# Kernel optimization log

Measured on AMD Instinct MI355X. Metric: run time of the kernel, lower is better.

## Reference

```python
import jax, jax.numpy as jnp
import numpy as np
from jax import lax


def conv3(x, w):
    # standard 3x3 conv, stride 1, pad 1, no bias (offset-predicting conv)
    return lax.conv_general_dilated(x, w, window_strides=(1, 1),
                                    padding=((1, 1), (1, 1)),
                                    dimension_numbers=('NCHW', 'OIHW', 'NCHW'))


def deform_conv(x, offset, weight, bias, groups):
    # torchvision.ops.DeformConv2d semantics, kernel 3x3, stride 1, pad 1,
    # dilation 1, conv groups == offset groups == `groups`.
    B, C, H, W = x.shape
    kH = kW = 3
    K = kH * kW
    pad = 1
    G = groups
    Cg = C // G
    outC = weight.shape[0]
    outCg = outC // G
    # offset layout: [B, G, K, 2(y,x), H, W]
    off = offset.reshape(B, G, K, 2, H, W)
    ky, kx = jnp.meshgrid(jnp.arange(kH, dtype=x.dtype),
                          jnp.arange(kW, dtype=x.dtype), indexing='ij')
    kyf = ky.reshape(K)
    kxf = kx.reshape(K)
    hg = jnp.arange(H, dtype=x.dtype) - pad
    wg = jnp.arange(W, dtype=x.dtype) - pad
    # sampling positions [B, G, K, H, W]
    py = off[:, :, :, 0] + hg[None, None, None, :, None] + kyf[None, None, :, None, None]
    px = off[:, :, :, 1] + wg[None, None, None, None, :] + kxf[None, None, :, None, None]
    y0 = jnp.floor(py)
    x0 = jnp.floor(px)
    wy = py - y0
    wx = px - x0
    xf = x.reshape(B, G, Cg, H * W)

    def gather(iy, ix):
        # bilinear corner gather with implicit zero padding
        valid = ((iy >= 0) & (iy < H) & (ix >= 0) & (ix < W)).astype(x.dtype)
        iyc = jnp.clip(iy, 0, H - 1).astype(jnp.int32)
        ixc = jnp.clip(ix, 0, W - 1).astype(jnp.int32)
        idx = (iyc * W + ixc).reshape(B, G, 1, K * H * W)
        idx = jnp.broadcast_to(idx, (B, G, Cg, K * H * W))
        v = jnp.take_along_axis(xf, idx, axis=3).reshape(B, G, Cg, K, H, W)
        return v * valid[:, :, None]

    one = jnp.asarray(1, x.dtype)
    val = ((one - wy) * (one - wx))[:, :, None] * gather(y0, x0) \
        + ((one - wy) * wx)[:, :, None] * gather(y0, x0 + 1) \
        + (wy * (one - wx))[:, :, None] * gather(y0 + 1, x0) \
        + (wy * wx)[:, :, None] * gather(y0 + 1, x0 + 1)
    # grouped conv as einsum over (Cg, K)
    wgrp = weight.reshape(G, outCg, Cg, K)
    out = jnp.einsum('bgckhw,gock->bgohw', val, wgrp).reshape(B, outC, H, W)
    return out + bias[None, :, None, None]


def setup_inputs() -> dict:
    key = jax.random.key(0)
    ks = jax.random.split(key, 16)
    B, C, H, W = 8, 64, 96, 96
    s = 0.01  # keep predicted offsets small / numerically tame
    fr = jax.random.normal(ks[0], (B, C, H, W), jnp.float32)
    ft = jax.random.normal(ks[1], (B, C, H, W), jnp.float32)
    # block 1: inC=128, 4 groups -> offset channels 72, deform weight [64, 32, 3, 3]
    off1_w = jax.random.normal(ks[2], (72, 128, 3, 3), jnp.float32) * s
    def1_w = jax.random.normal(ks[3], (64, 32, 3, 3), jnp.float32) * s
    def1_b = jax.random.normal(ks[4], (64,), jnp.float32) * s
    # blocks 2,3: inC=64, 4 groups
    off2_w = jax.random.normal(ks[5], (72, 64, 3, 3), jnp.float32) * s
    def2_w = jax.random.normal(ks[6], (64, 16, 3, 3), jnp.float32) * s
    def2_b = jax.random.normal(ks[7], (64,), jnp.float32) * s
    off3_w = jax.random.normal(ks[8], (72, 64, 3, 3), jnp.float32) * s
    def3_w = jax.random.normal(ks[9], (64, 16, 3, 3), jnp.float32) * s
    def3_b = jax.random.normal(ks[10], (64,), jnp.float32) * s
    # block 4: inC=64, 2 groups -> offset channels 36, deform weight [64, 32, 3, 3]
    off4_w = jax.random.normal(ks[11], (36, 64, 3, 3), jnp.float32) * s
    def4_w = jax.random.normal(ks[12], (64, 32, 3, 3), jnp.float32) * s
    def4_b = jax.random.normal(ks[13], (64,), jnp.float32) * s
    return {"fr": fr, "ft": ft,
            "off1_w": off1_w, "def1_w": def1_w, "def1_b": def1_b,
            "off2_w": off2_w, "def2_w": def2_w, "def2_b": def2_b,
            "off3_w": off3_w, "def3_w": def3_w, "def3_b": def3_b,
            "off4_w": off4_w, "def4_w": def4_w, "def4_b": def4_b}


def reference(fr, ft, off1_w, def1_w, def1_b, off2_w, def2_w, def2_b,
              off3_w, def3_w, def3_b, off4_w, def4_w, def4_b):
    cat_feat = jnp.concatenate((fr, ft), axis=1)            # [B, 2C, H, W]
    feat1 = deform_conv(cat_feat, conv3(cat_feat, off1_w), def1_w, def1_b, 4)
    feat2 = deform_conv(feat1, conv3(feat1, off2_w), def2_w, def2_b, 4)
    feat3 = deform_conv(feat2, conv3(feat2, off3_w), def3_w, def3_b, 4)
    # block 4: offsets predicted from feat3, sampling applied to ft
    aligned = deform_conv(ft, conv3(feat3, off4_w), def4_w, def4_b, 2)
    return aligned
```

## Files before the change

### kernel.cpp

```cpp
#include <hip/hip_runtime.h>
#include <hip/hip_bf16.h>


#define HH 96
#define WW 96
#define HWSZ (HH * WW)
#define BB 8
#define PW 98
#define PP (PW * PW)

using bf16x8 = __attribute__((ext_vector_type(8))) short;
using f32x4  = __attribute__((ext_vector_type(4))) float;

__device__ __forceinline__ unsigned int f2bf(float f) {
    __hip_bfloat16 h = __float2bfloat16(f);
    return (unsigned int)*reinterpret_cast<unsigned short*>(&h);
}
__device__ __forceinline__ float bf2f(unsigned short u) {
    return __uint_as_float(((unsigned int)u) << 16);
}

__global__ void prepack_w_kernel(const float* __restrict__ w, short* __restrict__ wp,
                                 int outC, int C, int MT, int KS) {
    int i = blockIdx.x * 256 + threadIdx.x;
    if (i >= MT * KS * 64) return;
    int lane = i & 63;
    int s = (i >> 6) % KS;
    int m = (i >> 6) / KS;
    int oc = m * 16 + (lane & 15);
    short v[8];
#pragma unroll
    for (int j = 0; j < 8; ++j) {
        int k = s * 32 + (lane >> 4) * 8 + j;
        int t = k / C, c = k % C;
        float f = (oc < outC) ? w[((size_t)oc * C + c) * 9 + t] : 0.f;
        v[j] = (short)f2bf(f);
    }
    *reinterpret_cast<bf16x8*>(wp + (size_t)i * 8) = *reinterpret_cast<bf16x8*>(v);
}

__global__ void pad_nhwc64_kernel(const float* __restrict__ src,
                                  __hip_bfloat16* __restrict__ out) {
    int i = blockIdx.x * 256 + threadIdx.x;
    if (i >= BB * PP) return;
    int px = i % PW, py = (i / PW) % PW, b = i / PP;
    unsigned int* op = reinterpret_cast<unsigned int*>(out + (size_t)i * 64);
    if (px == 0 || px == PW - 1 || py == 0 || py == PW - 1) {
#pragma unroll
        for (int c = 0; c < 32; ++c) op[c] = 0u;
        return;
    }
    const float* sp = src + (size_t)b * 64 * HWSZ + (py - 1) * WW + (px - 1);
#pragma unroll 8
    for (int c = 0; c < 32; ++c)
        op[c] = f2bf(sp[(size_t)(2 * c) * HWSZ]) | (f2bf(sp[(size_t)(2 * c + 1) * HWSZ]) << 16);
}

__global__ void padA_kernel(const __hip_bfloat16* __restrict__ src,
                            __hip_bfloat16* __restrict__ out) {
    int i = blockIdx.x * 256 + threadIdx.x;
    if (i >= BB * PP) return;
    int px = i % PW, py = (i / PW) % PW, b = i / PP;
    unsigned int* op = reinterpret_cast<unsigned int*>(out + (size_t)i * 64);
    if (px == 0 || px == PW - 1 || py == 0 || py == PW - 1) {
#pragma unroll
        for (int c = 0; c < 32; ++c) op[c] = 0u;
        return;
    }
    const unsigned short* sp = reinterpret_cast<const unsigned short*>(src)
        + (size_t)b * 64 * HWSZ + (py - 1) * WW + (px - 1);
#pragma unroll 8
    for (int c = 0; c < 32; ++c)
        op[c] = (unsigned int)sp[(size_t)(2 * c) * HWSZ]
              | ((unsigned int)sp[(size_t)(2 * c + 1) * HWSZ] << 16);
}

template <int C>
__global__ __launch_bounds__(256) void conv3_mfma_kernel(
    const __hip_bfloat16* __restrict__ xa,
    const __hip_bfloat16* __restrict__ xb,
    const short* __restrict__ wp,
    float* __restrict__ offb, int outC) {
    constexpr int KS = 9 * C / 32;
    int lane = threadIdx.x & 63;
    int wave = threadIdx.x >> 6;
    int y = blockIdx.x * 4 + wave;
    int m = blockIdx.y;
    int b = blockIdx.z;
    int l15 = lane & 15, lhi = lane >> 4;

    f32x4 acc[6];
#pragma unroll
    for (int nt = 0; nt < 6; ++nt) acc[nt] = (f32x4){0.f, 0.f, 0.f, 0.f};

    const short* wpm = wp + ((size_t)m * KS) * 64 * 8 + (size_t)lane * 8;

#pragma unroll 3
    for (int s = 0; s < KS; ++s) {
        bf16x8 afrag = *reinterpret_cast<const bf16x8*>(wpm + (size_t)s * 64 * 8);
        int t  = (s * 32) / C;
        int cb = (s * 32) % C;
        const __hip_bfloat16* xp = (cb < 64) ? xa : xb;
        int c0 = (cb & 63) + lhi * 8;
        int ky = t / 3, kx = t % 3;
        const short* bbase = reinterpret_cast<const short*>(xp)
            + (((size_t)b * PW + (y + ky)) * PW + kx + l15) * 64 + c0;
#pragma unroll
        for (int nt = 0; nt < 6; ++nt) {
            bf16x8 bfrag = *reinterpret_cast<const bf16x8*>(bbase + (size_t)nt * 16 * 64);
            acc[nt] = __builtin_amdgcn_mfma_f32_16x16x32_bf16(afrag, bfrag, acc[nt], 0, 0, 0);
        }
    }

    int ocb = m * 16 + lhi * 4;
#pragma unroll
    for (int nt = 0; nt < 6; ++nt) {
        int pix = y * WW + nt * 16 + l15;
#pragma unroll
        for (int r = 0; r < 4; ++r) {
            int oc = ocb + r;
            if (oc < outC)
                offb[((size_t)b * outC + oc) * HWSZ + pix] = acc[nt][r];
        }
    }
}

template <int CG, int OCG, int OFFC, bool SRCBF, bool DSTBF>
__global__ __launch_bounds__(256) void deform5_kernel(
    const void* __restrict__ xA, const void* __restrict__ xB,
    const float* __restrict__ offb,
    const float* __restrict__ w,
    const float* __restrict__ bias,
    __hip_bfloat16* __restrict__ anchw,
    float* __restrict__ outp) {
    int pix = blockIdx.x * 256 + threadIdx.x;
    int g   = blockIdx.y;
    int b   = blockIdx.z;
    int x = pix % WW, y = pix / WW;

    const float* offp = offb + ((size_t)b * OFFC + g * 18) * HWSZ + pix;

    float bw0[9], bw1[9], bw2[9], bw3[9];
    int   bi0[9], bi1[9], bi2[9], bi3[9];
#pragma unroll
    for (int k = 0; k < 9; ++k) {
        int ky = k / 3, kx = k % 3;
        float offy = offp[(size_t)(2 * k + 0) * HWSZ];
        float offx = offp[(size_t)(2 * k + 1) * HWSZ];
        float py = offy + (float)(y - 1 + ky);
        float px = offx + (float)(x - 1 + kx);
        float fy0 = floorf(py), fx0 = floorf(px);
        float wy = py - fy0, wx = px - fx0;
        int y0 = (int)fy0, x0 = (int)fx0;
        int y1 = y0 + 1,  x1 = x0 + 1;
        bool vy0 = (y0 >= 0) && (y0 < HH);
        bool vy1 = (y1 >= 0) && (y1 < HH);
        bool vx0 = (x0 >= 0) && (x0 < WW);
        bool vx1 = (x1 >= 0) && (x1 < WW);
        int cy0 = min(max(y0, 0), HH - 1), cy1 = min(max(y1, 0), HH - 1);
        int cx0 = min(max(x0, 0), WW - 1), cx1 = min(max(x1, 0), WW - 1);
        bw0[k] = (1.f - wy) * (1.f - wx) * ((vy0 && vx0) ? 1.f : 0.f);
        bw1[k] = (1.f - wy) * wx         * ((vy0 && vx1) ? 1.f : 0.f);
        bw2[k] = wy * (1.f - wx)         * ((vy1 && vx0) ? 1.f : 0.f);
        bw3[k] = wy * wx                 * ((vy1 && vx1) ? 1.f : 0.f);
        bi0[k] = cy0 * WW + cx0;  bi1[k] = cy0 * WW + cx1;
        bi2[k] = cy1 * WW + cx0;  bi3[k] = cy1 * WW + cx1;
    }

    float acc[OCG];
#pragma unroll
    for (int o = 0; o < OCG; ++o) acc[o] = bias[g * OCG + o];

    int gc = g * CG;
    const void* srcv = (gc < 64) ? xA : xB;
    size_t pbase = (size_t)b * 64 + (size_t)((gc < 64) ? gc : gc - 64);

    for (int c = 0; c < CG; ++c) {
        float v[9];
        if constexpr (SRCBF) {
            const unsigned short* p = (const unsigned short*)srcv + (pbase + c) * HWSZ;
#pragma unroll
            for (int k = 0; k < 9; ++k)
                v[k] = bw0[k] * bf2f(p[bi0[k]]) + bw1[k] * bf2f(p[bi1[k]])
                     + bw2[k] * bf2f(p[bi2[k]]) + bw3[k] * bf2f(p[bi3[k]]);
        } else {
            const float* p = (const float*)srcv + (pbase + c) * HWSZ;
#pragma unroll
            for (int k = 0; k < 9; ++k)
                v[k] = bw0[k] * p[bi0[k]] + bw1[k] * p[bi1[k]]
                     + bw2[k] * p[bi2[k]] + bw3[k] * p[bi3[k]];
        }
        const float* wc = w + ((size_t)(g * OCG) * CG + c) * 9;
#pragma unroll
        for (int o = 0; o < OCG; ++o) {
            const float* wo = wc + (size_t)o * CG * 9;
#pragma unroll
            for (int k = 0; k < 9; ++k) acc[o] = fmaf(v[k], wo[k], acc[o]);
        }
    }

    if constexpr (DSTBF) {
#pragma unroll
        for (int o = 0; o < OCG; ++o)
            *reinterpret_cast<unsigned short*>(
                anchw + ((size_t)b * 64 + g * OCG + o) * HWSZ + pix) =
                (unsigned short)f2bf(acc[o]);
    } else {
        float* op = outp + ((size_t)b * 64 + g * OCG) * HWSZ + pix;
#pragma unroll
        for (int o = 0; o < OCG; ++o) op[(size_t)o * HWSZ] = acc[o];
    }
}

extern "C" void kernel_launch(void* const* d_in, const int* in_sizes, int n_in,
                              void* d_out, int out_size, void* d_ws, size_t ws_size,
                              hipStream_t stream) {
    const float* fr     = (const float*)d_in[0];
    const float* ft     = (const float*)d_in[1];
    const float* off1_w = (const float*)d_in[2];
    const float* def1_w = (const float*)d_in[3];
    const float* def1_b = (const float*)d_in[4];
    const float* off2_w = (const float*)d_in[5];
    const float* def2_w = (const float*)d_in[6];
    const float* def2_b = (const float*)d_in[7];
    const float* off3_w = (const float*)d_in[8];
    const float* def3_w = (const float*)d_in[9];
    const float* def3_b = (const float*)d_in[10];
    const float* off4_w = (const float*)d_in[11];
    const float* def4_w = (const float*)d_in[12];
    const float* def4_b = (const float*)d_in[13];
    float* outp = (float*)d_out;

    char* ws = (char*)d_ws;
    const size_t offb_sz = (size_t)BB * 72 * HWSZ * 4;
    const size_t a_sz    = (size_t)BB * 64 * HWSZ * 2;
    const size_t p_sz    = (size_t)BB * PP * 64 * 2;
    float*          offb = (float*)ws;          ws += offb_sz;
    __hip_bfloat16* A1   = (__hip_bfloat16*)ws; ws += a_sz;
    __hip_bfloat16* P0   = (__hip_bfloat16*)ws; ws += p_sz;
    __hip_bfloat16* P1   = (__hip_bfloat16*)ws; ws += p_sz;
    short* wp1 = (short*)ws; ws += (size_t)5 * 36 * 64 * 8 * 2;
    short* wp2 = (short*)ws; ws += (size_t)5 * 18 * 64 * 8 * 2;
    short* wp3 = (short*)ws; ws += (size_t)5 * 18 * 64 * 8 * 2;
    short* wp4 = (short*)ws; ws += (size_t)3 * 18 * 64 * 8 * 2;
    __hip_bfloat16* A2 = P1;

    dim3 blk(256);
    int padBlocks = (BB * PP + 255) / 256;

    prepack_w_kernel<<<(5 * 36 * 64 + 255) / 256, blk, 0, stream>>>(off1_w, wp1, 72, 128, 5, 36);
    prepack_w_kernel<<<(5 * 18 * 64 + 255) / 256, blk, 0, stream>>>(off2_w, wp2, 72, 64, 5, 18);
    prepack_w_kernel<<<(5 * 18 * 64 + 255) / 256, blk, 0, stream>>>(off3_w, wp3, 72, 64, 5, 18);
    prepack_w_kernel<<<(3 * 18 * 64 + 255) / 256, blk, 0, stream>>>(off4_w, wp4, 36, 64, 3, 18);

    pad_nhwc64_kernel<<<padBlocks, blk, 0, stream>>>(fr, P0);
    pad_nhwc64_kernel<<<padBlocks, blk, 0, stream>>>(ft, P1);

    dim3 gDefG4(36, 4, BB), gDefG2(36, 2, BB);

    conv3_mfma_kernel<128><<<dim3(24, 5, BB), blk, 0, stream>>>(P0, P1, wp1, offb, 72);
    deform5_kernel<32, 16, 72, false, true><<<gDefG4, blk, 0, stream>>>(
        fr, ft, offb, def1_w, def1_b, A1, nullptr);

    padA_kernel<<<padBlocks, blk, 0, stream>>>(A1, P0);
    conv3_mfma_kernel<64><<<dim3(24, 5, BB), blk, 0, stream>>>(P0, P0, wp2, offb, 72);
    deform5_kernel<16, 16, 72, true, true><<<gDefG4, blk, 0, stream>>>(
        A1, A1, offb, def2_w, def2_b, A2, nullptr);

    padA_kernel<<<padBlocks, blk, 0, stream>>>(A2, P0);
    conv3_mfma_kernel<64><<<dim3(24, 5, BB), blk, 0, stream>>>(P0, P0, wp3, offb, 72);
    deform5_kernel<16, 16, 72, true, true><<<gDefG4, blk, 0, stream>>>(
        A2, A2, offb, def3_w, def3_b, A1, nullptr);

    padA_kernel<<<padBlocks, blk, 0, stream>>>(A1, P0);
    conv3_mfma_kernel<64><<<dim3(24, 3, BB), blk, 0, stream>>>(P0, P0, wp4, offb, 36);
    deform5_kernel<32, 32, 36, false, false><<<gDefG2, blk, 0, stream>>>(
        ft, ft, offb, def4_w, def4_b, nullptr, outp);
}
```

Baseline: 1.125 ms.

## Split deform conv channels across waves with LDS reduction; store offsets in bf16

The deformable conv kernel now assigns 64 pixels per block and splits the input-channel loop across the four waves. Partial sums are reduced through shared memory, and each wave writes a quarter of the output channels. This gives four times as many blocks, for more parallelism and latency hiding on the gather-heavy loop. The offset-conv output is also stored in bf16 instead of fp32, halving offset traffic at the cost of offset precision, which feeds floor() and can shift sampling positions.

```diff
diff --git a/kernel.cpp b/kernel.cpp
--- a/kernel.cpp
+++ b/kernel.cpp
@@ -80,7 +80,7 @@
     const __hip_bfloat16* __restrict__ xa,
     const __hip_bfloat16* __restrict__ xb,
     const short* __restrict__ wp,
-    float* __restrict__ offb, int outC) {
+    __hip_bfloat16* __restrict__ offb, int outC) {
     constexpr int KS = 9 * C / 32;
     int lane = threadIdx.x & 63;
     int wave = threadIdx.x >> 6;
@@ -120,33 +120,41 @@
         for (int r = 0; r < 4; ++r) {
             int oc = ocb + r;
             if (oc < outC)
-                offb[((size_t)b * outC + oc) * HWSZ + pix] = acc[nt][r];
+                *reinterpret_cast<unsigned short*>(
+                    offb + ((size_t)b * outC + oc) * HWSZ + pix) =
+                    (unsigned short)f2bf(acc[nt][r]);
         }
     }
 }
 
 template <int CG, int OCG, int OFFC, bool SRCBF, bool DSTBF>
-__global__ __launch_bounds__(256) void deform5_kernel(
+__global__ __launch_bounds__(256) void deform6_kernel(
     const void* __restrict__ xA, const void* __restrict__ xB,
-    const float* __restrict__ offb,
+    const __hip_bfloat16* __restrict__ offb,
     const float* __restrict__ w,
     const float* __restrict__ bias,
     __hip_bfloat16* __restrict__ anchw,
     float* __restrict__ outp) {
-    int pix = blockIdx.x * 256 + threadIdx.x;
-    int g   = blockIdx.y;
-    int b   = blockIdx.z;
+    constexpr int CC = CG / 4;
+    constexpr int Q  = OCG / 4;
+    __shared__ float lds[4][64][OCG + 1];
+
+    int wv   = threadIdx.x >> 6;
+    int lane = threadIdx.x & 63;
+    int pix  = blockIdx.x * 64 + lane;
+    int g    = blockIdx.y;
+    int b    = blockIdx.z;
     int x = pix % WW, y = pix / WW;
 
-    const float* offp = offb + ((size_t)b * OFFC + g * 18) * HWSZ + pix;
+    const __hip_bfloat16* ob = offb + ((size_t)b * OFFC + g * 18) * HWSZ + pix;
 
     float bw0[9], bw1[9], bw2[9], bw3[9];
     int   bi0[9], bi1[9], bi2[9], bi3[9];
 #pragma unroll
     for (int k = 0; k < 9; ++k) {
         int ky = k / 3, kx = k % 3;
-        float offy = offp[(size_t)(2 * k + 0) * HWSZ];
-        float offx = offp[(size_t)(2 * k + 1) * HWSZ];
+        float offy = bf2f(*reinterpret_cast<const unsigned short*>(ob + (size_t)(2 * k) * HWSZ));
+        float offx = bf2f(*reinterpret_cast<const unsigned short*>(ob + (size_t)(2 * k + 1) * HWSZ));
         float py = offy + (float)(y - 1 + ky);
         float px = offx + (float)(x - 1 + kx);
         float fy0 = floorf(py), fx0 = floorf(px);
@@ -169,13 +177,13 @@
 
     float acc[OCG];
 #pragma unroll
-    for (int o = 0; o < OCG; ++o) acc[o] = bias[g * OCG + o];
+    for (int o = 0; o < OCG; ++o) acc[o] = 0.f;
 
     int gc = g * CG;
     const void* srcv = (gc < 64) ? xA : xB;
-    size_t pbase = (size_t)b * 64 + (size_t)((gc < 64) ? gc : gc - 64);
-
-    for (int c = 0; c < CG; ++c) {
+    size_t pbase = (size_t)b * 64 + (size_t)((gc < 64) ? gc : gc - 64) + wv * CC;
+
+    for (int c = 0; c < CC; ++c) {
         float v[9];
         if constexpr (SRCBF) {
             const unsigned short* p = (const unsigned short*)srcv + (pbase + c) * HWSZ;
@@ -190,7 +198,7 @@
                 v[k] = bw0[k] * p[bi0[k]] + bw1[k] * p[bi1[k]]
                      + bw2[k] * p[bi2[k]] + bw3[k] * p[bi3[k]];
         }
-        const float* wc = w + ((size_t)(g * OCG) * CG + c) * 9;
+        const float* wc = w + ((size_t)(g * OCG) * CG + (wv * CC + c)) * 9;
 #pragma unroll
         for (int o = 0; o < OCG; ++o) {
             const float* wo = wc + (size_t)o * CG * 9;
@@ -199,16 +207,22 @@
         }
     }
 
-    if constexpr (DSTBF) {
-#pragma unroll
-        for (int o = 0; o < OCG; ++o)
+#pragma unroll
+    for (int o = 0; o < OCG; ++o) lds[wv][lane][o] = acc[o];
+    __syncthreads();
+
+#pragma unroll
+    for (int q = 0; q < Q; ++q) {
+        int o = wv * Q + q;
+        float s = lds[0][lane][o] + lds[1][lane][o] + lds[2][lane][o] + lds[3][lane][o]
+                + bias[g * OCG + o];
+        if constexpr (DSTBF) {
             *reinterpret_cast<unsigned short*>(
                 anchw + ((size_t)b * 64 + g * OCG + o) * HWSZ + pix) =
-                (unsigned short)f2bf(acc[o]);
-    } else {
-        float* op = outp + ((size_t)b * 64 + g * OCG) * HWSZ + pix;
-#pragma unroll
-        for (int o = 0; o < OCG; ++o) op[(size_t)o * HWSZ] = acc[o];
+                (unsigned short)f2bf(s);
+        } else {
+            outp[((size_t)b * 64 + g * OCG + o) * HWSZ + pix] = s;
+        }
     }
 }
 
@@ -232,10 +246,10 @@
     float* outp = (float*)d_out;
 
     char* ws = (char*)d_ws;
-    const size_t offb_sz = (size_t)BB * 72 * HWSZ * 4;
+    const size_t offb_sz = (size_t)BB * 72 * HWSZ * 2;
     const size_t a_sz    = (size_t)BB * 64 * HWSZ * 2;
     const size_t p_sz    = (size_t)BB * PP * 64 * 2;
-    float*          offb = (float*)ws;          ws += offb_sz;
+    __hip_bfloat16* offb = (__hip_bfloat16*)ws; ws += offb_sz;
     __hip_bfloat16* A1   = (__hip_bfloat16*)ws; ws += a_sz;
     __hip_bfloat16* P0   = (__hip_bfloat16*)ws; ws += p_sz;
     __hip_bfloat16* P1   = (__hip_bfloat16*)ws; ws += p_sz;
@@ -256,24 +270,24 @@
     pad_nhwc64_kernel<<<padBlocks, blk, 0, stream>>>(fr, P0);
     pad_nhwc64_kernel<<<padBlocks, blk, 0, stream>>>(ft, P1);
 
-    dim3 gDefG4(36, 4, BB), gDefG2(36, 2, BB);
+    dim3 gDefG4(144, 4, BB), gDefG2(144, 2, BB);
 
     conv3_mfma_kernel<128><<<dim3(24, 5, BB), blk, 0, stream>>>(P0, P1, wp1, offb, 72);
-    deform5_kernel<32, 16, 72, false, true><<<gDefG4, blk, 0, stream>>>(
+    deform6_kernel<32, 16, 72, false, true><<<gDefG4, blk, 0, stream>>>(
         fr, ft, offb, def1_w, def1_b, A1, nullptr);
 
     padA_kernel<<<padBlocks, blk, 0, stream>>>(A1, P0);
     conv3_mfma_kernel<64><<<dim3(24, 5, BB), blk, 0, stream>>>(P0, P0, wp2, offb, 72);
-    deform5_kernel<16, 16, 72, true, true><<<gDefG4, blk, 0, stream>>>(
+    deform6_kernel<16, 16, 72, true, true><<<gDefG4, blk, 0, stream>>>(
         A1, A1, offb, def2_w, def2_b, A2, nullptr);
 
     padA_kernel<<<padBlocks, blk, 0, stream>>>(A2, P0);
     conv3_mfma_kernel<64><<<dim3(24, 5, BB), blk, 0, stream>>>(P0, P0, wp3, offb, 72);
-    deform5_kernel<16, 16, 72, true, true><<<gDefG4, blk, 0, stream>>>(
+    deform6_kernel<16, 16, 72, true, true><<<gDefG4, blk, 0, stream>>>(
         A2, A2, offb, def3_w, def3_b, A1, nullptr);
 
     padA_kernel<<<padBlocks, blk, 0, stream>>>(A1, P0);
     conv3_mfma_kernel<64><<<dim3(24, 3, BB), blk, 0, stream>>>(P0, P0, wp4, offb, 36);
-    deform5_kernel<32, 32, 36, false, false><<<gDefG2, blk, 0, stream>>>(
+    deform6_kernel<32, 32, 36, false, false><<<gDefG2, blk, 0, stream>>>(
         ft, ft, offb, def4_w, def4_b, nullptr, outp);
 }
```

Result: slower. 1.699 ms (+51.0%).
